# Kernel tuning notes

Measured on AMD Instinct MI355X. Metric: run time of the kernel, lower is better.

Reference implementation:

```python
import jax, jax.numpy as jnp
import numpy as np

B, C, H, W = 8, 128, 48, 48
RED = 16  # SELayer reduction


def setup_inputs() -> dict:
    key = jax.random.key(0)
    ks = jax.random.split(key, 8)
    s = 0.05  # weight scale for numerical stability of softmax
    return {
        "x": jax.random.normal(ks[0], (B, C, H, W), jnp.float32),
        "Wq": jax.random.normal(ks[1], (C, C), jnp.float32) * s,
        "bq": jnp.zeros((C,), jnp.float32),
        "Wk": jax.random.normal(ks[2], (C, C), jnp.float32) * s,
        "bk": jnp.zeros((C,), jnp.float32),
        "Wv": jax.random.normal(ks[3], (C, C), jnp.float32) * s,
        "bv": jnp.zeros((C,), jnp.float32),
        "se_w1": jax.random.normal(ks[4], (C // RED, C), jnp.float32) * s,
        "se_w2": jax.random.normal(ks[5], (C, C // RED), jnp.float32) * s,
        "gamma": jax.random.normal(ks[6], (1,), jnp.float32),
    }


def reference(x, Wq, bq, Wk, bk, Wv, bv, se_w1, se_w2, gamma):
    b, c, h, w = x.shape
    n = h * w
    xf = x.reshape(b, c, n)  # (B, C, N)
    # 1x1 convs == per-pixel linear maps over channels
    q = jnp.einsum('oc,bcn->bon', Wq, xf) + bq[None, :, None]  # (B, C, N)
    k = jnp.einsum('oc,bcn->bon', Wk, xf) + bk[None, :, None]
    v = jnp.einsum('oc,bcn->bon', Wv, xf) + bv[None, :, None]
    # energy[b, i, j] = sum_c q[b, c, i] * k[b, c, j]  (unscaled, as in source)
    energy = jnp.einsum('bci,bcj->bij', q, k)  # (B, N, N)
    attn = jax.nn.softmax(energy, axis=-1)
    # out[b, c, i] = sum_j v[b, c, j] * attn[b, i, j]
    out = jnp.einsum('bcj,bij->bci', v, attn).reshape(b, c, h, w)
    # SELayer applied to the input x
    y = jnp.mean(x, axis=(2, 3))  # (B, C) global average pool
    y = jax.nn.relu(y @ se_w1.T)  # (B, C//RED)
    y = jax.nn.sigmoid(y @ se_w2.T)  # (B, C)
    x_se = x * y[:, :, None, None]
    return gamma[0] * out + x_se
```

## Files before the change

### kernel.cpp

```cpp
#include <hip/hip_runtime.h>

typedef _Float16 half8 __attribute__((ext_vector_type(8)));
typedef _Float16 half4 __attribute__((ext_vector_type(4)));
typedef _Float16 half2v __attribute__((ext_vector_type(2)));
typedef float f32x4 __attribute__((ext_vector_type(4)));

#define BATCH 8
#define CH 128
#define NPIX 2304
#define SPLIT 6
#define JPER (NPIX / SPLIT)
#define NT (JPER / 64)
#define BN (BATCH * NPIX)
#define LOG2E 1.44269504088896f

__device__ __forceinline__ f32x4 mfma32(half8 a, half8 b, f32x4 c) {
    return __builtin_amdgcn_mfma_f32_16x16x32_f16(a, b, c, 0, 0, 0);
}
__device__ __forceinline__ f32x4 mfma16(half4 a, half4 b, f32x4 c) {
    return __builtin_amdgcn_mfma_f32_16x16x16f16(a, b, c, 0, 0, 0);
}

__global__ __launch_bounds__(256) void k_prep(
        const float* __restrict__ x, const float* __restrict__ Wq,
        const float* __restrict__ Wk, const float* __restrict__ Wv,
        _Float16* __restrict__ Wh, float* __restrict__ y0) {
    const int bid = blockIdx.x;
    const int t = threadIdx.x;
    if (bid < 1024) {
        const int row = bid;
        const float4* p = (const float4*)(x + (size_t)row * NPIX);
        float s = 0.f;
        for (int tt = t; tt < NPIX / 4; tt += 256) {
            float4 v = p[tt];
            s += v.x + v.y + v.z + v.w;
        }
        for (int m = 1; m < 64; m <<= 1) s += __shfl_xor(s, m);
        __shared__ float ls[4];
        if ((t & 63) == 0) ls[t >> 6] = s;
        __syncthreads();
        if (t == 0) y0[row] = (ls[0] + ls[1] + ls[2] + ls[3]) * (1.0f / (float)NPIX);
    } else {
        int i = (bid - 1024) * 256 + t;
        const float* src = (i < 16384) ? Wq : ((i < 32768) ? Wk : Wv);
        Wh[i] = (_Float16)src[i & 16383];
    }
}

__global__ __launch_bounds__(256) void k_proj(
        const float* __restrict__ x, const _Float16* __restrict__ Wh,
        const float* __restrict__ bq, const float* __restrict__ bk, const float* __restrict__ bv,
        _Float16* __restrict__ qT, _Float16* __restrict__ kT, _Float16* __restrict__ vN,
        const float* __restrict__ y0, const float* __restrict__ se_w1,
        const float* __restrict__ se_w2, float* __restrict__ scale) {
    const int which = blockIdx.z;
    const int t = threadIdx.x;

    if (which == 3) {
        if (blockIdx.x != 0 || blockIdx.y != 0) return;
        __shared__ float ly[128];
        __shared__ float ly1[8];
        for (int b = 0; b < BATCH; ++b) {
            if (t < 128) ly[t] = y0[b * 128 + t];
            __syncthreads();
            if (t < 8) {
                float a = 0.f;
                for (int c = 0; c < 128; ++c) a += se_w1[t * 128 + c] * ly[c];
                ly1[t] = fmaxf(a, 0.f);
            }
            __syncthreads();
            if (t < 128) {
                float a = 0.f;
                for (int r = 0; r < 8; ++r) a += se_w2[t * 8 + r] * ly1[r];
                scale[b * 128 + t] = 1.f / (1.f + __expf(-a));
            }
            __syncthreads();
        }
        return;
    }

    const int n0 = blockIdx.x * 128;
    const int b = blockIdx.y;
    const float* bias = (which == 0) ? bq : ((which == 1) ? bk : bv);
    const _Float16* W = Wh + which * 16384;

    __shared__ __align__(16) _Float16 xt[128 * 128];

    {
        const float* xb = x + (size_t)b * CH * NPIX + n0;
        for (int rep = 0; rep < 8; ++rep) {
            int flat = rep * 256 + t;
            int c2 = (flat >> 5) * 2;
            int n4 = (flat & 31) * 4;
            float4 va = *(const float4*)(xb + (size_t)c2 * NPIX + n4);
            float4 vb = *(const float4*)(xb + (size_t)(c2 + 1) * NPIX + n4);
            int cc = c2 & 7, ck = c2 >> 3;
            *(half2v*)(xt + (n4 + 0) * 128 + ((ck ^ ((n4 + 0) & 7)) * 8) + cc) =
                (half2v){(_Float16)va.x, (_Float16)vb.x};
            *(half2v*)(xt + (n4 + 1) * 128 + ((ck ^ ((n4 + 1) & 7)) * 8) + cc) =
                (half2v){(_Float16)va.y, (_Float16)vb.y};
            *(half2v*)(xt + (n4 + 2) * 128 + ((ck ^ ((n4 + 2) & 7)) * 8) + cc) =
                (half2v){(_Float16)va.z, (_Float16)vb.z};
            *(half2v*)(xt + (n4 + 3) * 128 + ((ck ^ ((n4 + 3) & 7)) * 8) + cc) =
                (half2v){(_Float16)va.w, (_Float16)vb.w};
        }
    }
    __syncthreads();

    const int lane = t & 63, w = t >> 6;
    const int ln15 = lane & 15, quad = lane >> 4;

    f32x4 zero4 = {0.f, 0.f, 0.f, 0.f};
    f32x4 acc[8][2];
    for (int mt = 0; mt < 8; ++mt) { acc[mt][0] = zero4; acc[mt][1] = zero4; }

    for (int ks = 0; ks < 4; ++ks) {
        half8 bf[2];
        for (int nt = 0; nt < 2; ++nt) {
            int row = w * 32 + nt * 16 + ln15;
            int ch = ks * 4 + quad;
            bf[nt] = *(const half8*)(xt + row * 128 + ((ch ^ (row & 7)) * 8));
        }
        for (int mt = 0; mt < 8; ++mt) {
            half8 af = *(const half8*)(W + (mt * 16 + ln15) * 128 + ks * 32 + quad * 8);
            acc[mt][0] = mfma32(af, bf[0], acc[mt][0]);
            acc[mt][1] = mfma32(af, bf[1], acc[mt][1]);
        }
    }
    __syncthreads();

    if (which == 2) {
        for (int mt = 0; mt < 8; ++mt)
            for (int nt = 0; nt < 2; ++nt)
                for (int r = 0; r < 4; ++r) {
                    int c = mt * 16 + quad * 4 + r;
                    int nl = w * 32 + nt * 16 + ln15;
                    xt[c * 128 + (((nl >> 3) ^ (c & 7)) * 8) + (nl & 7)] =
                        (_Float16)(acc[mt][nt][r] + bias[c]);
                }
        __syncthreads();
        _Float16* vb = vN + (size_t)b * CH * NPIX + n0;
        for (int rep = 0; rep < 8; ++rep) {
            int c = rep * 16 + (t >> 4), ch = t & 15;
            *(half8*)(vb + (size_t)c * NPIX + ch * 8) =
                *(const half8*)(xt + c * 128 + ((ch ^ (c & 7)) * 8));
        }
    } else {
        for (int mt = 0; mt < 8; ++mt)
            for (int nt = 0; nt < 2; ++nt)
                for (int r = 0; r < 4; r += 2) {
                    int c = mt * 16 + quad * 4 + r;
                    int nl = w * 32 + nt * 16 + ln15;
                    *(half2v*)(xt + nl * 128 + (((c >> 3) ^ (nl & 7)) * 8) + (c & 7)) =
                        (half2v){(_Float16)(acc[mt][nt][r] + bias[c]),
                                 (_Float16)(acc[mt][nt][r + 1] + bias[c + 1])};
                }
        __syncthreads();
        _Float16* dst = ((which == 0) ? qT : kT) + ((size_t)b * NPIX + n0) * CH;
        for (int rep = 0; rep < 8; ++rep) {
            int nl = rep * 16 + (t >> 4), ch = t & 15;
            *(half8*)(dst + nl * 128 + ch * 8) =
                *(const half8*)(xt + nl * 128 + ((ch ^ (nl & 7)) * 8));
        }
    }
}

__global__ __launch_bounds__(256, 2) void k_attn(
        const _Float16* __restrict__ qT, const _Float16* __restrict__ kT,
        const _Float16* __restrict__ vN,
        _Float16* __restrict__ o_part, float* __restrict__ g_m, float* __restrict__ g_l) {
    const int i0 = blockIdx.x * 128;
    const int b = blockIdx.y;
    const int split = blockIdx.z;
    const int t = threadIdx.x;
    const int lane = t & 63, w = t >> 6;
    const int ln15 = lane & 15, quad = lane >> 4;

    __shared__ __align__(16) _Float16 sh[16384];
    _Float16* k_s = sh;
    _Float16* v_s = sh + 8192;

    half8 qf[2][4];
    #pragma unroll
    for (int ih = 0; ih < 2; ++ih) {
        const _Float16* qb = qT + ((size_t)b * NPIX + i0 + w * 32 + ih * 16 + ln15) * CH + quad * 8;
        #pragma unroll
        for (int kc = 0; kc < 4; ++kc) qf[ih][kc] = *(const half8*)(qb + kc * 32);
    }

    f32x4 zero4 = {0.f, 0.f, 0.f, 0.f};
    f32x4 os[2][8];
    #pragma unroll
    for (int ih = 0; ih < 2; ++ih)
        for (int ct = 0; ct < 8; ++ct) os[ih][ct] = zero4;
    float m[2] = {-1e30f, -1e30f}, l[2] = {0.f, 0.f};

    for (int it = 0; it < NT; ++it) {
        const int j0 = split * JPER + it * 64;
        __syncthreads();
        {
            const _Float16* kb = kT + ((size_t)b * NPIX + j0) * CH;
            for (int rep = 0; rep < 4; ++rep) {
                int row = rep * 16 + (t >> 4), ch = t & 15;
                *(half8*)(k_s + row * 128 + ((ch ^ (row & 7)) * 8)) =
                    *(const half8*)(kb + row * CH + ch * 8);
            }
        }
        {
            const _Float16* vb = vN + (size_t)b * CH * NPIX + j0;
            for (int rep = 0; rep < 4; ++rep) {
                int c = rep * 32 + (t >> 3), ch = t & 7;
                *(half8*)(v_s + c * 64 + ((ch ^ (c & 7)) * 8)) =
                    *(const half8*)(vb + (size_t)c * NPIX + ch * 8);
            }
        }
        __syncthreads();

        f32x4 s[2][4];
        #pragma unroll
        for (int jt = 0; jt < 4; ++jt) { s[0][jt] = zero4; s[1][jt] = zero4; }
        #pragma unroll
        for (int jt = 0; jt < 4; ++jt) {
            #pragma unroll
            for (int kc = 0; kc < 4; ++kc) {
                int row = jt * 16 + ln15, ch = kc * 4 + quad;
                half8 kf = *(const half8*)(k_s + row * 128 + ((ch ^ (row & 7)) * 8));
                s[0][jt] = mfma32(kf, qf[0][kc], s[0][jt]);
                s[1][jt] = mfma32(kf, qf[1][kc], s[1][jt]);
            }
        }

        half4 pf[2][4];
        #pragma unroll
        for (int ih = 0; ih < 2; ++ih) {
            float mx = fmaxf(fmaxf(s[ih][0][0], s[ih][0][1]), fmaxf(s[ih][0][2], s[ih][0][3]));
            #pragma unroll
            for (int jt = 1; jt < 4; ++jt)
                mx = fmaxf(mx, fmaxf(fmaxf(s[ih][jt][0], s[ih][jt][1]),
                                     fmaxf(s[ih][jt][2], s[ih][jt][3])));
            mx = fmaxf(mx, __shfl_xor(mx, 16));
            mx = fmaxf(mx, __shfl_xor(mx, 32));
            float mnew = fmaxf(m[ih], mx);
            float alpha = exp2f((m[ih] - mnew) * LOG2E);
            m[ih] = mnew;
            float mbias = mnew * LOG2E;

            float sum = 0.f;
            #pragma unroll
            for (int jt = 0; jt < 4; ++jt)
                #pragma unroll
                for (int r = 0; r < 4; ++r) {
                    float p = exp2f(fmaf(s[ih][jt][r], LOG2E, -mbias));
                    sum += p;
                    pf[ih][jt][r] = (_Float16)p;
                }
            sum += __shfl_xor(sum, 16);
            sum += __shfl_xor(sum, 32);
            l[ih] = l[ih] * alpha + sum;

            #pragma unroll
            for (int ct = 0; ct < 8; ++ct) {
                os[ih][ct][0] *= alpha; os[ih][ct][1] *= alpha;
                os[ih][ct][2] *= alpha; os[ih][ct][3] *= alpha;
            }
        }

        #pragma unroll
        for (int ct = 0; ct < 8; ++ct) {
            int c = ct * 16 + ln15;
            #pragma unroll
            for (int jt = 0; jt < 4; ++jt) {
                int chunk = jt * 2 + (quad >> 1);
                half4 vf = *(const half4*)(v_s + c * 64 + ((chunk ^ (c & 7)) * 8) + (quad & 1) * 4);
                os[0][ct] = mfma16(vf, pf[0][jt], os[0][ct]);
                os[1][ct] = mfma16(vf, pf[1][jt], os[1][ct]);
            }
        }
    }

    if (quad == 0) {
        #pragma unroll
        for (int ih = 0; ih < 2; ++ih) {
            int i = i0 + w * 32 + ih * 16 + ln15;
            g_m[(size_t)(split * BATCH + b) * NPIX + i] = m[ih];
            g_l[(size_t)(split * BATCH + b) * NPIX + i] = l[ih];
        }
    }
    __syncthreads();
    #pragma unroll
    for (int ih = 0; ih < 2; ++ih)
        #pragma unroll
        for (int ct = 0; ct < 8; ++ct)
            #pragma unroll
            for (int r = 0; r < 4; ++r) {
                int c = ct * 16 + quad * 4 + r;
                int il = w * 32 + ih * 16 + ln15;
                int chunk = il >> 3;
                sh[c * 128 + ((chunk ^ (c & 7)) * 8) + (il & 7)] = (_Float16)os[ih][ct][r];
            }
    __syncthreads();
    _Float16* op = o_part + (size_t)(split * BATCH + b) * CH * NPIX;
    for (int rep = 0; rep < 8; ++rep) {
        int c = rep * 16 + (t >> 4), ch = t & 15;
        *(half8*)(op + (size_t)c * NPIX + i0 + ch * 8) =
            *(const half8*)(sh + c * 128 + ((ch ^ (c & 7)) * 8));
    }
}

__global__ __launch_bounds__(256) void k_combine(
        const _Float16* __restrict__ o_part, const float* __restrict__ g_m,
        const float* __restrict__ g_l, const float* __restrict__ x,
        const float* __restrict__ scale, const float* __restrict__ gamma_p,
        float* __restrict__ out) {
    const int i0 = blockIdx.x * 64;
    const int b = blockIdx.y;
    const int t = threadIdx.x;
    __shared__ float wl[SPLIT][64];

    if (t < 64) {
        int i = i0 + t;
        float mm[SPLIT], llv[SPLIT];
        float M = -1e30f;
        for (int s = 0; s < SPLIT; ++s) {
            mm[s] = g_m[(size_t)(s * BATCH + b) * NPIX + i];
            llv[s] = g_l[(size_t)(s * BATCH + b) * NPIX + i];
            M = fmaxf(M, mm[s]);
        }
        float L = 0.f, e[SPLIT];
        for (int s = 0; s < SPLIT; ++s) {
            e[s] = exp2f((mm[s] - M) * LOG2E);
            L += e[s] * llv[s];
        }
        float inv = 1.f / L;
        for (int s = 0; s < SPLIT; ++s) wl[s][t] = e[s] * inv;
    }
    __syncthreads();

    const float g = gamma_p[0];
    for (int rep = 0; rep < 4; ++rep) {
        int c = rep * 32 + (t >> 3), i8 = (t & 7) * 8;
        size_t base = ((size_t)b * CH + c) * NPIX + i0 + i8;
        float acc[8] = {0.f, 0.f, 0.f, 0.f, 0.f, 0.f, 0.f, 0.f};
        for (int s = 0; s < SPLIT; ++s) {
            half8 o = *(const half8*)(o_part +
                ((size_t)(s * BATCH + b) * CH + c) * NPIX + i0 + i8);
            for (int e = 0; e < 8; ++e) acc[e] += wl[s][i8 + e] * (float)o[e];
        }
        float sc = scale[b * 128 + c];
        float4 x0 = *(const float4*)(x + base);
        float4 x1 = *(const float4*)(x + base + 4);
        float4 r0, r1;
        r0.x = g * acc[0] + x0.x * sc; r0.y = g * acc[1] + x0.y * sc;
        r0.z = g * acc[2] + x0.z * sc; r0.w = g * acc[3] + x0.w * sc;
        r1.x = g * acc[4] + x1.x * sc; r1.y = g * acc[5] + x1.y * sc;
        r1.z = g * acc[6] + x1.z * sc; r1.w = g * acc[7] + x1.w * sc;
        *(float4*)(out + base) = r0;
        *(float4*)(out + base + 4) = r1;
    }
}

extern "C" void kernel_launch(void* const* d_in, const int* in_sizes, int n_in,
                              void* d_out, int out_size, void* d_ws, size_t ws_size,
                              hipStream_t stream) {
    const float* x     = (const float*)d_in[0];
    const float* Wq    = (const float*)d_in[1];
    const float* bq    = (const float*)d_in[2];
    const float* Wk    = (const float*)d_in[3];
    const float* bk    = (const float*)d_in[4];
    const float* Wv    = (const float*)d_in[5];
    const float* bv    = (const float*)d_in[6];
    const float* se_w1 = (const float*)d_in[7];
    const float* se_w2 = (const float*)d_in[8];
    const float* gamma = (const float*)d_in[9];
    float* out = (float*)d_out;

    char* ws = (char*)d_ws;
    const size_t E = (size_t)BATCH * NPIX * CH;
    _Float16* qT = (_Float16*)(ws);
    _Float16* kT = (_Float16*)(ws + E * 2);
    _Float16* vN = (_Float16*)(ws + E * 4);
    _Float16* op = (_Float16*)(ws + E * 6);
    char* tail   = ws + E * 6 + (size_t)SPLIT * E * 2;
    _Float16* Wh = (_Float16*)(tail);
    float* g_m   = (float*)(tail + 98304);
    float* g_l   = (float*)(tail + 98304 + (size_t)SPLIT * BN * 4);
    float* y0    = (float*)(tail + 98304 + 2 * (size_t)SPLIT * BN * 4);
    float* scale = (float*)(tail + 98304 + 2 * (size_t)SPLIT * BN * 4 + 4096);

    k_prep<<<1216, 256, 0, stream>>>(x, Wq, Wk, Wv, Wh, y0);
    k_proj<<<dim3(NPIX / 128, BATCH, 4), 256, 0, stream>>>(
        x, Wh, bq, bk, bv, qT, kT, vN, y0, se_w1, se_w2, scale);
    k_attn<<<dim3(NPIX / 128, BATCH, SPLIT), 256, 0, stream>>>(
        qT, kT, vN, op, g_m, g_l);
    k_combine<<<dim3(NPIX / 64, BATCH), 256, 0, stream>>>(
        op, g_m, g_l, x, scale, gamma, out);
}
```

Measured before the change: 153.0 us.

## Fuse SE pooling into projection and SE MLP into combine kernel

Removes the separate pass over x that computed per-channel means in k_prep. The sums are now accumulated with shared and global atomics while k_proj loads x for the Q projection, and y0 is zeroed by a memset first. The serial single-block SE MLP in k_proj is dropped; each k_combine block recomputes the small MLP for its batch and splits channels over a new z dimension of 4. This saves a full read of x and a serialized tail block, but adds atomics, redundant MLP work per block and an extra memset launch.

```diff
diff --git a/kernel.cpp b/kernel.cpp
--- a/kernel.cpp
+++ b/kernel.cpp
@@ -22,69 +22,32 @@
 }
 
 __global__ __launch_bounds__(256) void k_prep(
-        const float* __restrict__ x, const float* __restrict__ Wq,
-        const float* __restrict__ Wk, const float* __restrict__ Wv,
-        _Float16* __restrict__ Wh, float* __restrict__ y0) {
-    const int bid = blockIdx.x;
-    const int t = threadIdx.x;
-    if (bid < 1024) {
-        const int row = bid;
-        const float4* p = (const float4*)(x + (size_t)row * NPIX);
-        float s = 0.f;
-        for (int tt = t; tt < NPIX / 4; tt += 256) {
-            float4 v = p[tt];
-            s += v.x + v.y + v.z + v.w;
-        }
-        for (int m = 1; m < 64; m <<= 1) s += __shfl_xor(s, m);
-        __shared__ float ls[4];
-        if ((t & 63) == 0) ls[t >> 6] = s;
-        __syncthreads();
-        if (t == 0) y0[row] = (ls[0] + ls[1] + ls[2] + ls[3]) * (1.0f / (float)NPIX);
-    } else {
-        int i = (bid - 1024) * 256 + t;
-        const float* src = (i < 16384) ? Wq : ((i < 32768) ? Wk : Wv);
-        Wh[i] = (_Float16)src[i & 16383];
-    }
+        const float* __restrict__ Wq, const float* __restrict__ Wk,
+        const float* __restrict__ Wv, _Float16* __restrict__ Wh) {
+    int i = blockIdx.x * 256 + threadIdx.x;
+    const float* src = (i < 16384) ? Wq : ((i < 32768) ? Wk : Wv);
+    Wh[i] = (_Float16)src[i & 16383];
 }
 
 __global__ __launch_bounds__(256) void k_proj(
         const float* __restrict__ x, const _Float16* __restrict__ Wh,
         const float* __restrict__ bq, const float* __restrict__ bk, const float* __restrict__ bv,
         _Float16* __restrict__ qT, _Float16* __restrict__ kT, _Float16* __restrict__ vN,
-        const float* __restrict__ y0, const float* __restrict__ se_w1,
-        const float* __restrict__ se_w2, float* __restrict__ scale) {
+        float* __restrict__ y0) {
     const int which = blockIdx.z;
     const int t = threadIdx.x;
-
-    if (which == 3) {
-        if (blockIdx.x != 0 || blockIdx.y != 0) return;
-        __shared__ float ly[128];
-        __shared__ float ly1[8];
-        for (int b = 0; b < BATCH; ++b) {
-            if (t < 128) ly[t] = y0[b * 128 + t];
-            __syncthreads();
-            if (t < 8) {
-                float a = 0.f;
-                for (int c = 0; c < 128; ++c) a += se_w1[t * 128 + c] * ly[c];
-                ly1[t] = fmaxf(a, 0.f);
-            }
-            __syncthreads();
-            if (t < 128) {
-                float a = 0.f;
-                for (int r = 0; r < 8; ++r) a += se_w2[t * 8 + r] * ly1[r];
-                scale[b * 128 + t] = 1.f / (1.f + __expf(-a));
-            }
-            __syncthreads();
-        }
-        return;
-    }
-
     const int n0 = blockIdx.x * 128;
     const int b = blockIdx.y;
     const float* bias = (which == 0) ? bq : ((which == 1) ? bk : bv);
     const _Float16* W = Wh + which * 16384;
 
     __shared__ __align__(16) _Float16 xt[128 * 128];
+    __shared__ float ysum[128];
+
+    if (which == 0) {
+        if (t < 128) ysum[t] = 0.f;
+        __syncthreads();
+    }
 
     {
         const float* xb = x + (size_t)b * CH * NPIX + n0;
@@ -94,6 +57,10 @@
             int n4 = (flat & 31) * 4;
             float4 va = *(const float4*)(xb + (size_t)c2 * NPIX + n4);
             float4 vb = *(const float4*)(xb + (size_t)(c2 + 1) * NPIX + n4);
+            if (which == 0) {
+                atomicAdd(&ysum[c2],     va.x + va.y + va.z + va.w);
+                atomicAdd(&ysum[c2 + 1], vb.x + vb.y + vb.z + vb.w);
+            }
             int cc = c2 & 7, ck = c2 >> 3;
             *(half2v*)(xt + (n4 + 0) * 128 + ((ck ^ ((n4 + 0) & 7)) * 8) + cc) =
                 (half2v){(_Float16)va.x, (_Float16)vb.x};
@@ -106,6 +73,9 @@
         }
     }
     __syncthreads();
+
+    if (which == 0 && t < 128)
+        atomicAdd(&y0[b * 128 + t], ysum[t]);
 
     const int lane = t & 63, w = t >> 6;
     const int ln15 = lane & 15, quad = lane >> 4;
@@ -310,13 +280,18 @@
 __global__ __launch_bounds__(256) void k_combine(
         const _Float16* __restrict__ o_part, const float* __restrict__ g_m,
         const float* __restrict__ g_l, const float* __restrict__ x,
-        const float* __restrict__ scale, const float* __restrict__ gamma_p,
+        const float* __restrict__ y0, const float* __restrict__ se_w1,
+        const float* __restrict__ se_w2, const float* __restrict__ gamma_p,
         float* __restrict__ out) {
     const int i0 = blockIdx.x * 64;
     const int b = blockIdx.y;
     const int t = threadIdx.x;
     __shared__ float wl[SPLIT][64];
-
+    __shared__ float ly[128];
+    __shared__ float ly1[8];
+    __shared__ float scs[32];
+
+    if (t < 128) ly[t] = y0[b * 128 + t] * (1.0f / (float)NPIX);
     if (t < 64) {
         int i = i0 + t;
         float mm[SPLIT], llv[SPLIT];
@@ -335,10 +310,23 @@
         for (int s = 0; s < SPLIT; ++s) wl[s][t] = e[s] * inv;
     }
     __syncthreads();
+    if (t < 8) {
+        float a = 0.f;
+        for (int c = 0; c < 128; ++c) a += se_w1[t * 128 + c] * ly[c];
+        ly1[t] = fmaxf(a, 0.f);
+    }
+    __syncthreads();
+    if (t < 32) {
+        int c = blockIdx.z * 32 + t;
+        float a = 0.f;
+        for (int r = 0; r < 8; ++r) a += se_w2[c * 8 + r] * ly1[r];
+        scs[t] = 1.f / (1.f + __expf(-a));
+    }
+    __syncthreads();
 
     const float g = gamma_p[0];
-    for (int rep = 0; rep < 4; ++rep) {
-        int c = rep * 32 + (t >> 3), i8 = (t & 7) * 8;
+    {
+        int c = blockIdx.z * 32 + (t >> 3), i8 = (t & 7) * 8;
         size_t base = ((size_t)b * CH + c) * NPIX + i0 + i8;
         float acc[8] = {0.f, 0.f, 0.f, 0.f, 0.f, 0.f, 0.f, 0.f};
         for (int s = 0; s < SPLIT; ++s) {
@@ -346,7 +334,7 @@
                 ((size_t)(s * BATCH + b) * CH + c) * NPIX + i0 + i8);
             for (int e = 0; e < 8; ++e) acc[e] += wl[s][i8 + e] * (float)o[e];
         }
-        float sc = scale[b * 128 + c];
+        float sc = scs[t >> 3];
         float4 x0 = *(const float4*)(x + base);
         float4 x1 = *(const float4*)(x + base + 4);
         float4 r0, r1;
@@ -385,13 +373,13 @@
     float* g_m   = (float*)(tail + 98304);
     float* g_l   = (float*)(tail + 98304 + (size_t)SPLIT * BN * 4);
     float* y0    = (float*)(tail + 98304 + 2 * (size_t)SPLIT * BN * 4);
-    float* scale = (float*)(tail + 98304 + 2 * (size_t)SPLIT * BN * 4 + 4096);
-
-    k_prep<<<1216, 256, 0, stream>>>(x, Wq, Wk, Wv, Wh, y0);
-    k_proj<<<dim3(NPIX / 128, BATCH, 4), 256, 0, stream>>>(
-        x, Wh, bq, bk, bv, qT, kT, vN, y0, se_w1, se_w2, scale);
+
+    hipMemsetAsync(y0, 0, 1024 * sizeof(float), stream);
+    k_prep<<<192, 256, 0, stream>>>(Wq, Wk, Wv, Wh);
+    k_proj<<<dim3(NPIX / 128, BATCH, 3), 256, 0, stream>>>(
+        x, Wh, bq, bk, bv, qT, kT, vN, y0);
     k_attn<<<dim3(NPIX / 128, BATCH, SPLIT), 256, 0, stream>>>(
         qT, kT, vN, op, g_m, g_l);
-    k_combine<<<dim3(NPIX / 64, BATCH), 256, 0, stream>>>(
-        op, g_m, g_l, x, scale, gamma, out);
-}
+    k_combine<<<dim3(NPIX / 64, BATCH, 4), 256, 0, stream>>>(
+        op, g_m, g_l, x, y0, se_w1, se_w2, gamma, out);
+}
```

New measurement: 159.0 us. 1.04x slower.
